# Kernel optimization log

Hardware: AMD Instinct MI355X
Metric: run time of the kernel (lower is better)

Reference implementation:

```python
import jax, jax.numpy as jnp
import numpy as np

B, T, D, U = 32, 2048, 512, 512

def setup_inputs() -> dict:
    key = jax.random.key(0)
    ks = jax.random.split(key, 8)
    s = 0.02
    return {
        "query": jax.random.normal(ks[0], (B, D), dtype=jnp.float32),
        "values": jax.random.normal(ks[1], (B, T, D), dtype=jnp.float32),
        "W1_w": jax.random.normal(ks[2], (D, U), dtype=jnp.float32) * s,
        "W1_b": jnp.zeros((U,), dtype=jnp.float32),
        "W2_w": jax.random.normal(ks[3], (D, U), dtype=jnp.float32) * s,
        "W2_b": jnp.zeros((U,), dtype=jnp.float32),
        "V_w": jax.random.normal(ks[4], (U, 1), dtype=jnp.float32) * s,
        "V_b": jnp.zeros((1,), dtype=jnp.float32),
    }

def reference(query, values, W1_w, W1_b, W2_w, W2_b, V_w, V_b):
    # query: [B, D] -> [B, 1, U]; values: [B, T, D] -> [B, T, U]
    q_proj = (query @ W1_w + W1_b)[:, None, :]              # [B, 1, U]
    v_proj = jnp.einsum('btd,du->btu', values, W2_w) + W2_b  # [B, T, U]
    score = jnp.tanh(q_proj + v_proj) @ V_w + V_b            # [B, T, 1]
    attn = jax.nn.softmax(score, axis=1)                     # [B, T, 1]
    context = jnp.sum(attn * values, axis=1)                 # [B, D]
    return context, attn
```

## Files before the change

kernel.cpp:

```cpp
#include <hip/hip_runtime.h>
#include <hip/hip_bf16.h>
#include <cstddef>
#include <cstdint>

#define B_ 32
#define T_ 2048
#define D_ 512
#define U_ 512

typedef __attribute__((ext_vector_type(8))) short bf16x8;
typedef __attribute__((ext_vector_type(4))) float f32x4;

__device__ __forceinline__ unsigned short f2bf(float f) {
  union { float f; unsigned u; } x; x.f = f;
  unsigned r = x.u + 0x7fffu + ((x.u >> 16) & 1u);
  return (unsigned short)(r >> 16);
}
__device__ __forceinline__ float tanh_fast(float x) {
  float e = __expf(2.0f * x);
  return 1.0f - 2.0f * __builtin_amdgcn_rcpf(e + 1.0f);
}

#define AS1C(p) ((const __attribute__((address_space(1))) unsigned*)(p))
#define AS3(p)  ((__attribute__((address_space(3))) unsigned*)(p))

__device__ __forceinline__ void wave0_sumabs_vw(const float* __restrict__ Vw,
                                                float* Cs, int tid) {
  if (tid < 64) {
    float c = 0.f;
    #pragma unroll
    for (int i = 0; i < 8; ++i) c += fabsf(Vw[tid + i * 64]);
    c += __shfl_xor(c, 1);  c += __shfl_xor(c, 2);  c += __shfl_xor(c, 4);
    c += __shfl_xor(c, 8);  c += __shfl_xor(c, 16); c += __shfl_xor(c, 32);
    if (tid == 0) *Cs = c;
  }
}

__global__ void kA_prep(const float* __restrict__ W2, unsigned* __restrict__ W2P,
                        const float* __restrict__ query, const float* __restrict__ W1,
                        const float* __restrict__ W1b, const float* __restrict__ W2b,
                        float* __restrict__ qp, float* __restrict__ ctx) {
  const int tid = threadIdx.x;
  if (blockIdx.x < 64) {
    const int kg = blockIdx.x >> 2, q4 = blockIdx.x & 3;
    __shared__ unsigned short w2s[8][514];
    const float4* W2v = (const float4*)(W2 + (size_t)(kg * 32 + q4 * 8) * U_);
    #pragma unroll
    for (int i = 0; i < 4; ++i) {
      int idx4 = i * 256 + tid;
      float4 v = W2v[idx4];
      int r = idx4 >> 7, c = (idx4 & 127) * 4;
      w2s[r][c + 0] = f2bf(v.x); w2s[r][c + 1] = f2bf(v.y);
      w2s[r][c + 2] = f2bf(v.z); w2s[r][c + 3] = f2bf(v.w);
    }
    __syncthreads();
    const int idx = tid & 63;
    const int lr = (idx >> 2) & 15, j = idx & 3;
    const int kb = j * 2;
    #pragma unroll
    for (int r = 0; r < 8; ++r) {
      int ut = r * 4 + (tid >> 6);
      W2P[ut * 4096 + kg * 256 + q4 * 64 + idx] =
          (unsigned)w2s[kb][ut * 16 + lr] | ((unsigned)w2s[kb + 1][ut * 16 + lr] << 16);
    }
  } else {
    __shared__ float qs[D_];
    __shared__ float red[4][64];
    const int blk2 = blockIdx.x - 64;
    const int b = blk2 >> 3, us = blk2 & 7;
    const int ul = tid & 63, dq = tid >> 6;
    const int u = us * 64 + ul;
    qs[tid] = query[b * D_ + tid];
    qs[tid + 256] = query[b * D_ + tid + 256];
    __syncthreads();
    float a0 = 0, a1 = 0, a2 = 0, a3 = 0;
    const int d0 = dq * 128;
    for (int d = 0; d < 128; d += 4) {
      a0 += qs[d0 + d + 0] * W1[(size_t)(d0 + d + 0) * U_ + u];
      a1 += qs[d0 + d + 1] * W1[(size_t)(d0 + d + 1) * U_ + u];
      a2 += qs[d0 + d + 2] * W1[(size_t)(d0 + d + 2) * U_ + u];
      a3 += qs[d0 + d + 3] * W1[(size_t)(d0 + d + 3) * U_ + u];
    }
    red[dq][ul] = (a0 + a1) + (a2 + a3);
    __syncthreads();
    if (dq == 0) {
      float s = red[0][ul] + red[1][ul] + red[2][ul] + red[3][ul];
      qp[b * U_ + u] = s + W1b[u] + W2b[u];
    }
    if (tid < 64) ctx[blk2 * 64 + tid] = 0.0f;
  }
}

__global__ __launch_bounds__(1024, 4) void k2attn(
    const float* __restrict__ values, const unsigned short* __restrict__ W2P,
    const float* __restrict__ qp, const float* __restrict__ Vw,
    float* __restrict__ score, float* __restrict__ ctxU) {
  __shared__ __align__(16) float av[3][4096];
  __shared__ float sred[16][32];
  __shared__ float ps2[64];
  __shared__ float pc[512];
  __shared__ float Cs;

  const int tid = threadIdx.x;
  const int bx = blockIdx.x;
  const int m0 = bx * 64;
  const int b = m0 >> 11;
  const int l = tid & 63, w = tid >> 6;
  const int lr = l & 15, lq = l >> 4;
  const int h = w >> 3, uw = w & 7;

  const int row_g = w * 4 + (l >> 4);
  const int qsw = (l & 15) ^ (row_g & 15);
  const float* vsrc = values + (size_t)(m0 + row_g) * D_ + qsw * 4;

  f32x4 acc[2][4];
  #pragma unroll
  for (int mi = 0; mi < 2; ++mi)
    #pragma unroll
    for (int ni = 0; ni < 4; ++ni) acc[mi][ni] = (f32x4){0.f, 0.f, 0.f, 0.f};

  const unsigned short* Bb = W2P + (size_t)(uw * 4) * 8192 + (size_t)l * 8;

  auto stage = [&](int s) {
    __builtin_amdgcn_global_load_lds(AS1C(vsrc + s * 64), AS3(&av[s % 3][w * 256]), 16, 0, 0);
  };
  bf16x8 Bf[3][4];
  auto loadB = [&](int slot, int kappa) {
    #pragma unroll
    for (int ni = 0; ni < 4; ++ni)
      Bf[slot][ni] = *(const bf16x8*)(Bb + (size_t)ni * 8192 + (size_t)kappa * 512);
  };

  wave0_sumabs_vw(Vw, &Cs, tid);

  loadB(0, 0);
  loadB(1, 1);
  stage(0);
  stage(1);
  __builtin_amdgcn_sched_barrier(0);
  asm volatile("s_waitcnt vmcnt(1) lgkmcnt(0)" ::: "memory");
  __builtin_amdgcn_s_barrier();
  __builtin_amdgcn_sched_barrier(0);
  const float C = Cs;

  #pragma unroll
  for (int e = 0; e < 8; ++e) {
    const float* buf = (const float*)av[e % 3];
    #pragma unroll
    for (int kq = 0; kq < 2; ++kq) {
      const int kappa = e * 2 + kq;
      if (kappa + 2 < 16) loadB((kappa + 2) % 3, kappa + 2);
      __builtin_amdgcn_sched_barrier(0);
      const int p0 = (kq * 8 + lq * 2) ^ lr;
      #pragma unroll
      for (int mi = 0; mi < 2; ++mi) {
        const int row = h * 32 + mi * 16 + lr;
        f32x4 flo = *(const f32x4*)&buf[row * 64 + (p0 << 2)];
        f32x4 fhi = *(const f32x4*)&buf[row * 64 + ((p0 ^ 1) << 2)];
        union { bf16x8 v; __hip_bfloat162 hh[4]; } A;
        A.hh[0] = __float22bfloat162_rn(make_float2(flo.x, flo.y));
        A.hh[1] = __float22bfloat162_rn(make_float2(flo.z, flo.w));
        A.hh[2] = __float22bfloat162_rn(make_float2(fhi.x, fhi.y));
        A.hh[3] = __float22bfloat162_rn(make_float2(fhi.z, fhi.w));
        __builtin_amdgcn_s_setprio(1);
        acc[mi][0] = __builtin_amdgcn_mfma_f32_16x16x32_bf16(A.v, Bf[kappa % 3][0], acc[mi][0], 0, 0, 0);
        acc[mi][1] = __builtin_amdgcn_mfma_f32_16x16x32_bf16(A.v, Bf[kappa % 3][1], acc[mi][1], 0, 0, 0);
        acc[mi][2] = __builtin_amdgcn_mfma_f32_16x16x32_bf16(A.v, Bf[kappa % 3][2], acc[mi][2], 0, 0, 0);
        acc[mi][3] = __builtin_amdgcn_mfma_f32_16x16x32_bf16(A.v, Bf[kappa % 3][3], acc[mi][3], 0, 0, 0);
        __builtin_amdgcn_s_setprio(0);
      }
    }
    if (e + 2 < 8) stage(e + 2);
    __builtin_amdgcn_sched_barrier(0);
    if (e < 7) {
      if (e == 6) asm volatile("s_waitcnt vmcnt(8)" ::: "memory");
      else        asm volatile("s_waitcnt vmcnt(9)" ::: "memory");
      __builtin_amdgcn_s_barrier();
      __builtin_amdgcn_sched_barrier(0);
    }
  }

  float sacc[2][4];
  #pragma unroll
  for (int mi = 0; mi < 2; ++mi)
    #pragma unroll
    for (int r = 0; r < 4; ++r) sacc[mi][r] = 0.0f;
  #pragma unroll
  for (int ni = 0; ni < 4; ++ni) {
    int u = (uw * 4 + ni) * 16 + lr;
    float qpv = qp[b * U_ + u], vv = Vw[u];
    #pragma unroll
    for (int mi = 0; mi < 2; ++mi)
      #pragma unroll
      for (int r = 0; r < 4; ++r)
        sacc[mi][r] += tanh_fast(acc[mi][ni][r] + qpv) * vv;
  }
  #pragma unroll
  for (int mi = 0; mi < 2; ++mi)
    #pragma unroll
    for (int r = 0; r < 4; ++r) {
      float v = sacc[mi][r];
      v += __shfl_xor(v, 1); v += __shfl_xor(v, 2);
      v += __shfl_xor(v, 4); v += __shfl_xor(v, 8);
      if (lr == 0) sred[w][mi * 16 + lq * 4 + r] = v;
    }
  __syncthreads();

  if (tid < 64) {
    const int hh = tid >> 5, loc = tid & 31;
    float s = 0.f;
    #pragma unroll
    for (int j = 0; j < 8; ++j) s += sred[hh * 8 + j][loc];
    score[m0 + tid] = s;
    ps2[tid] = __expf(s - C);
  }
  __syncthreads();

  const int col = tid & 511, rh = tid >> 9;
  float accc = 0.f;
  #pragma unroll 4
  for (int row = 0; row < 32; ++row)
    accc += ps2[rh * 32 + row] * values[(size_t)(m0 + rh * 32 + row) * D_ + col];
  if (rh == 1) pc[col] = accc;
  __syncthreads();
  if (rh == 0) atomicAdd(&ctxU[(size_t)b * D_ + col], accc + pc[col]);
}

__global__ void kB_final(const float* __restrict__ Vw, float* __restrict__ attn,
                         float* __restrict__ ctx) {
  __shared__ float Cs;
  __shared__ float red[4];
  const int b = blockIdx.x, tid = threadIdx.x;
  wave0_sumabs_vw(Vw, &Cs, tid);
  __syncthreads();
  const float C = Cs;
  float* s = attn + b * T_;
  float p[8];
  float sum = 0.f;
  #pragma unroll
  for (int i = 0; i < 8; ++i) { p[i] = __expf(s[tid + i * 256] - C); sum += p[i]; }
  #pragma unroll
  for (int off = 1; off < 64; off <<= 1) sum += __shfl_xor(sum, off);
  if ((tid & 63) == 0) red[tid >> 6] = sum;
  __syncthreads();
  sum = (red[0] + red[1]) + (red[2] + red[3]);
  const float inv = 1.0f / sum;
  #pragma unroll
  for (int i = 0; i < 8; ++i) attn[b * T_ + tid + i * 256] = p[i] * inv;
  #pragma unroll
  for (int i = 0; i < 2; ++i) ctx[b * D_ + tid + i * 256] *= inv;
}

extern "C" void kernel_launch(void* const* d_in, const int* in_sizes, int n_in,
                              void* d_out, int out_size, void* d_ws, size_t ws_size,
                              hipStream_t stream) {
  const float* query = (const float*)d_in[0];
  const float* values = (const float*)d_in[1];
  const float* W1w = (const float*)d_in[2];
  const float* W1b = (const float*)d_in[3];
  const float* W2w = (const float*)d_in[4];
  const float* W2b = (const float*)d_in[5];
  const float* Vw  = (const float*)d_in[6];

  float* out = (float*)d_out;
  float* ctx  = out;
  float* attn = out + B_ * D_;
  float* score = attn;

  char* ws = (char*)d_ws;
  unsigned* W2P = (unsigned*)ws;
  float* qp    = (float*)(ws + 512 * 1024);

  kA_prep<<<320, 256, 0, stream>>>(W2w, W2P, query, W1w, W1b, W2b, qp, ctx);
  k2attn<<<1024, 1024, 0, stream>>>(values, (const unsigned short*)W2P, qp, Vw, score, ctx);
  kB_final<<<32, 256, 0, stream>>>(Vw, attn, ctx);
}
```

Before: 268.5 us.

## Shrink attention tile to 32 rows with 512-thread blocks and simpler double buffering

Halves the attention kernel's row tile from 64 to 32 rows, moving to 512-thread blocks on a 2048-block grid. Each of the 8 waves now owns 64 U columns for all 32 rows. The hand-scheduled triple-buffered LDS pipeline with explicit vmcnt waits and setprio is replaced by a plain __syncthreads double buffer and register double-buffered B fragments. The aim is to cut LDS use and raise occupancy. In exchange, the W2 fragments are reloaded twice as often per row, there are twice as many context atomics, and memory/compute overlap is less finely controlled.

```diff
diff --git a/kernel.cpp b/kernel.cpp
--- a/kernel.cpp
+++ b/kernel.cpp
@@ -91,27 +91,25 @@
   }
 }
 
-__global__ __launch_bounds__(1024, 4) void k2attn(
+__global__ __launch_bounds__(512, 4) void k2attn(
     const float* __restrict__ values, const unsigned short* __restrict__ W2P,
     const float* __restrict__ qp, const float* __restrict__ Vw,
     float* __restrict__ score, float* __restrict__ ctxU) {
-  __shared__ __align__(16) float av[3][4096];
-  __shared__ float sred[16][32];
-  __shared__ float ps2[64];
-  __shared__ float pc[512];
+  __shared__ __align__(16) float av[2][2048];
+  __shared__ float sred[8][32];
+  __shared__ float ps2[32];
   __shared__ float Cs;
 
   const int tid = threadIdx.x;
   const int bx = blockIdx.x;
-  const int m0 = bx * 64;
+  const int m0 = bx * 32;
   const int b = m0 >> 11;
   const int l = tid & 63, w = tid >> 6;
   const int lr = l & 15, lq = l >> 4;
-  const int h = w >> 3, uw = w & 7;
-
-  const int row_g = w * 4 + (l >> 4);
-  const int qsw = (l & 15) ^ (row_g & 15);
-  const float* vsrc = values + (size_t)(m0 + row_g) * D_ + qsw * 4;
+
+  const int row_st = tid >> 4;
+  const int qsw = (tid & 15) ^ (row_st & 15);
+  const float* vsrc = values + (size_t)(m0 + row_st) * D_ + qsw * 4;
 
   f32x4 acc[2][4];
   #pragma unroll
@@ -119,65 +117,52 @@
     #pragma unroll
     for (int ni = 0; ni < 4; ++ni) acc[mi][ni] = (f32x4){0.f, 0.f, 0.f, 0.f};
 
-  const unsigned short* Bb = W2P + (size_t)(uw * 4) * 8192 + (size_t)l * 8;
-
-  auto stage = [&](int s) {
-    __builtin_amdgcn_global_load_lds(AS1C(vsrc + s * 64), AS3(&av[s % 3][w * 256]), 16, 0, 0);
+  const unsigned short* Bb = W2P + (size_t)(w * 4) * 8192 + (size_t)l * 8;
+
+  auto stage = [&](int e, int p) {
+    __builtin_amdgcn_global_load_lds(AS1C(vsrc + e * 64), AS3(&av[p][w * 256]), 16, 0, 0);
   };
-  bf16x8 Bf[3][4];
-  auto loadB = [&](int slot, int kappa) {
+
+  wave0_sumabs_vw(Vw, &Cs, tid);
+
+  bf16x8 Bc[4], Bn[4];
+  stage(0, 0);
+  #pragma unroll
+  for (int ni = 0; ni < 4; ++ni) Bc[ni] = *(const bf16x8*)(Bb + (size_t)ni * 8192);
+
+  for (int kg = 0; kg < 16; ++kg) {
+    const int e = kg >> 1, p = e & 1;
+    if ((kg & 1) == 0) {
+      __syncthreads();
+      if (e < 7) stage(e + 1, p ^ 1);
+    }
+    if (kg < 15) {
+      #pragma unroll
+      for (int ni = 0; ni < 4; ++ni)
+        Bn[ni] = *(const bf16x8*)(Bb + (size_t)ni * 8192 + (size_t)(kg + 1) * 512);
+    }
+    const int kq = kg & 1;
+    const int p0 = (kq * 8 + lq * 2) ^ lr;
+    bf16x8 a[2];
+    #pragma unroll
+    for (int mi = 0; mi < 2; ++mi) {
+      const int row = mi * 16 + lr;
+      f32x4 flo = *(const f32x4*)&av[p][row * 64 + (p0 << 2)];
+      f32x4 fhi = *(const f32x4*)&av[p][row * 64 + ((p0 ^ 1) << 2)];
+      union { bf16x8 v; __hip_bfloat162 h[4]; } A;
+      A.h[0] = __float22bfloat162_rn(make_float2(flo.x, flo.y));
+      A.h[1] = __float22bfloat162_rn(make_float2(flo.z, flo.w));
+      A.h[2] = __float22bfloat162_rn(make_float2(fhi.x, fhi.y));
+      A.h[3] = __float22bfloat162_rn(make_float2(fhi.z, fhi.w));
+      a[mi] = A.v;
+    }
     #pragma unroll
     for (int ni = 0; ni < 4; ++ni)
-      Bf[slot][ni] = *(const bf16x8*)(Bb + (size_t)ni * 8192 + (size_t)kappa * 512);
-  };
-
-  wave0_sumabs_vw(Vw, &Cs, tid);
-
-  loadB(0, 0);
-  loadB(1, 1);
-  stage(0);
-  stage(1);
-  __builtin_amdgcn_sched_barrier(0);
-  asm volatile("s_waitcnt vmcnt(1) lgkmcnt(0)" ::: "memory");
-  __builtin_amdgcn_s_barrier();
-  __builtin_amdgcn_sched_barrier(0);
-  const float C = Cs;
-
-  #pragma unroll
-  for (int e = 0; e < 8; ++e) {
-    const float* buf = (const float*)av[e % 3];
-    #pragma unroll
-    for (int kq = 0; kq < 2; ++kq) {
-      const int kappa = e * 2 + kq;
-      if (kappa + 2 < 16) loadB((kappa + 2) % 3, kappa + 2);
-      __builtin_amdgcn_sched_barrier(0);
-      const int p0 = (kq * 8 + lq * 2) ^ lr;
       #pragma unroll
-      for (int mi = 0; mi < 2; ++mi) {
-        const int row = h * 32 + mi * 16 + lr;
-        f32x4 flo = *(const f32x4*)&buf[row * 64 + (p0 << 2)];
-        f32x4 fhi = *(const f32x4*)&buf[row * 64 + ((p0 ^ 1) << 2)];
-        union { bf16x8 v; __hip_bfloat162 hh[4]; } A;
-        A.hh[0] = __float22bfloat162_rn(make_float2(flo.x, flo.y));
-        A.hh[1] = __float22bfloat162_rn(make_float2(flo.z, flo.w));
-        A.hh[2] = __float22bfloat162_rn(make_float2(fhi.x, fhi.y));
-        A.hh[3] = __float22bfloat162_rn(make_float2(fhi.z, fhi.w));
-        __builtin_amdgcn_s_setprio(1);
-        acc[mi][0] = __builtin_amdgcn_mfma_f32_16x16x32_bf16(A.v, Bf[kappa % 3][0], acc[mi][0], 0, 0, 0);
-        acc[mi][1] = __builtin_amdgcn_mfma_f32_16x16x32_bf16(A.v, Bf[kappa % 3][1], acc[mi][1], 0, 0, 0);
-        acc[mi][2] = __builtin_amdgcn_mfma_f32_16x16x32_bf16(A.v, Bf[kappa % 3][2], acc[mi][2], 0, 0, 0);
-        acc[mi][3] = __builtin_amdgcn_mfma_f32_16x16x32_bf16(A.v, Bf[kappa % 3][3], acc[mi][3], 0, 0, 0);
-        __builtin_amdgcn_s_setprio(0);
-      }
-    }
-    if (e + 2 < 8) stage(e + 2);
-    __builtin_amdgcn_sched_barrier(0);
-    if (e < 7) {
-      if (e == 6) asm volatile("s_waitcnt vmcnt(8)" ::: "memory");
-      else        asm volatile("s_waitcnt vmcnt(9)" ::: "memory");
-      __builtin_amdgcn_s_barrier();
-      __builtin_amdgcn_sched_barrier(0);
-    }
+      for (int mi = 0; mi < 2; ++mi)
+        acc[mi][ni] = __builtin_amdgcn_mfma_f32_16x16x32_bf16(a[mi], Bc[ni], acc[mi][ni], 0, 0, 0);
+    #pragma unroll
+    for (int ni = 0; ni < 4; ++ni) Bc[ni] = Bn[ni];
   }
 
   float sacc[2][4];
@@ -187,7 +172,7 @@
     for (int r = 0; r < 4; ++r) sacc[mi][r] = 0.0f;
   #pragma unroll
   for (int ni = 0; ni < 4; ++ni) {
-    int u = (uw * 4 + ni) * 16 + lr;
+    int u = (w * 4 + ni) * 16 + lr;
     float qpv = qp[b * U_ + u], vv = Vw[u];
     #pragma unroll
     for (int mi = 0; mi < 2; ++mi)
@@ -206,24 +191,21 @@
     }
   __syncthreads();
 
-  if (tid < 64) {
-    const int hh = tid >> 5, loc = tid & 31;
+  if (tid < 32) {
     float s = 0.f;
     #pragma unroll
-    for (int j = 0; j < 8; ++j) s += sred[hh * 8 + j][loc];
+    for (int wv = 0; wv < 8; ++wv) s += sred[wv][tid];
     score[m0 + tid] = s;
-    ps2[tid] = __expf(s - C);
-  }
-  __syncthreads();
-
-  const int col = tid & 511, rh = tid >> 9;
+    ps2[tid] = __expf(s - Cs);
+  }
+  __syncthreads();
+
   float accc = 0.f;
+  const int col = tid;
   #pragma unroll 4
   for (int row = 0; row < 32; ++row)
-    accc += ps2[rh * 32 + row] * values[(size_t)(m0 + rh * 32 + row) * D_ + col];
-  if (rh == 1) pc[col] = accc;
-  __syncthreads();
-  if (rh == 0) atomicAdd(&ctxU[(size_t)b * D_ + col], accc + pc[col]);
+    accc += ps2[row] * values[(size_t)(m0 + row) * D_ + col];
+  atomicAdd(&ctxU[(size_t)b * D_ + col], accc);
 }
 
 __global__ void kB_final(const float* __restrict__ Vw, float* __restrict__ attn,
@@ -272,6 +254,6 @@
   float* qp    = (float*)(ws + 512 * 1024);
 
   kA_prep<<<320, 256, 0, stream>>>(W2w, W2P, query, W1w, W1b, W2b, qp, ctx);
-  k2attn<<<1024, 1024, 0, stream>>>(values, (const unsigned short*)W2P, qp, Vw, score, ctx);
+  k2attn<<<2048, 512, 0, stream>>>(values, (const unsigned short*)W2P, qp, Vw, score, ctx);
   kB_final<<<32, 256, 0, stream>>>(Vw, attn, ctx);
 }
```

New measurement: 262.6 us. 1.02x faster.
